# Optimization experiments

Measured on AMD Instinct MI355X. Metric: run time of the kernel, lower is better.

Reference implementation:

```python
import jax, jax.numpy as jnp
from jax import lax
import numpy as np

N_INPUTS = 256
N_REGS = 256
BATCH = 4096
T = 64  # num_clk_cycles


def setup_inputs() -> dict:
    key = jax.random.key(0)
    k1, k2, k3 = jax.random.split(key, 3)
    P = jax.random.normal(k1, (N_INPUTS, BATCH, T), dtype=jnp.float32)
    wa = jax.random.randint(k2, (N_REGS,), 0, N_INPUTS + N_REGS, dtype=jnp.int32)
    wb = jax.random.randint(k3, (N_REGS,), 0, N_INPUTS + N_REGS, dtype=jnp.int32)
    return {"P": P, "wa": wa, "wb": wb}


def reference(P, wa, wb):
    # PIEmbedding: clamp params to [-2,2], sigmoid(4*param[:, idx]) per cycle.
    # Precompute all cycles at once: X[t, b, i] in (0,1).
    X = jax.nn.sigmoid(4.0 * jnp.clip(P, -2.0, 2.0))          # [n_inputs, B, T]
    X = jnp.transpose(X, (2, 1, 0))                            # [T, B, n_inputs]
    B = P.shape[1]

    # Representative exec-generated soft sequential circuit:
    # each of N_REGS gates is a soft XOR of two signals drawn from
    # concat([primary_inputs, registers]); gate outputs become next registers.
    def step(states, x_t):
        sig = jnp.concatenate([x_t, states], axis=-1)          # [B, n_inputs+n_regs]
        a = sig[:, wa]                                          # [B, n_regs]
        b = sig[:, wb]
        new_states = a + b - 2.0 * a * b                        # soft XOR
        return new_states, None

    init = jnp.full((B, N_REGS), 0.5, dtype=P.dtype)            # init_registers()
    out, _ = lax.scan(step, init, X)                            # scan over clk cycles
    return out                                                  # [B, n_regs]
```

## Files before the change

kernel.cpp:

```cpp
#include <hip/hip_runtime.h>

#define N_IN   256
#define N_REG  256
#define NBATCH 4096
#define TT     64
#define TC     32
#define NCHUNK (TT / TC)
#define TILE_LD 257

__global__ __launch_bounds__(256, 4) void circuit_scan(
    const float* __restrict__ P,
    const int*   __restrict__ wa,
    const int*   __restrict__ wb,
    float*       __restrict__ out)
{
    __shared__ float tile[TC][TILE_LD];
    __shared__ float st0[N_REG];
    __shared__ float st1[N_REG];

    const int tid = threadIdx.x;
    const int b   = blockIdx.x;

    const int  ia   = wa[tid];
    const int  ib   = wb[tid];
    const bool a_in = ia < N_IN;
    const bool b_in = ib < N_IN;
    const int  ia_m = a_in ? ia : (ia - N_IN);
    const int  ib_m = b_in ? ib : (ib - N_IN);

    st0[tid] = 0.5f;

    const int row = tid >> 3;
    const int q   = tid & 7;

    float4 regs[8];

    #pragma unroll
    for (int it = 0; it < 8; ++it) {
        const int r = it * 32 + row;
        regs[it] = *reinterpret_cast<const float4*>(
            P + (size_t)r * (NBATCH * TT) + (size_t)b * TT + q * 4);
    }

    float mystate = 0.5f;

    for (int c = 0; c < NCHUNK; ++c) {
        #pragma unroll
        for (int it = 0; it < 8; ++it) {
            const int r = it * 32 + row;
            float xv[4] = {regs[it].x, regs[it].y, regs[it].z, regs[it].w};
            #pragma unroll
            for (int j = 0; j < 4; ++j) {
                float x = xv[j];
                x = fminf(2.0f, fmaxf(-2.0f, x));
                float s = 1.0f / (1.0f + __expf(-4.0f * x));
                tile[q * 4 + j][r] = s;
            }
        }
        if (c + 1 < NCHUNK) {
            const int t0 = (c + 1) * TC;
            #pragma unroll
            for (int it = 0; it < 8; ++it) {
                const int r = it * 32 + row;
                regs[it] = *reinterpret_cast<const float4*>(
                    P + (size_t)r * (NBATCH * TT) + (size_t)b * TT + t0 + q * 4);
            }
        }
        __syncthreads();

        #pragma unroll
        for (int tl = 0; tl < TC; ++tl) {
            const float* sread  = (tl & 1) ? st1 : st0;
            float*       swrite = (tl & 1) ? st0 : st1;
            const float* arow   = &tile[tl][0];
            float a  = *(a_in ? (arow + ia_m) : (sread + ia_m));
            float bb = *(b_in ? (arow + ib_m) : (sread + ib_m));
            float ns = a + bb - 2.0f * a * bb;
            swrite[tid] = ns;
            mystate = ns;
            __syncthreads();
        }
    }

    out[(size_t)b * N_REG + tid] = mystate;
}

extern "C" void kernel_launch(void* const* d_in, const int* in_sizes, int n_in,
                              void* d_out, int out_size, void* d_ws, size_t ws_size,
                              hipStream_t stream) {
    const float* P  = (const float*)d_in[0];
    const int*   wa = (const int*)d_in[1];
    const int*   wb = (const int*)d_in[2];
    float*       out = (float*)d_out;
    circuit_scan<<<NBATCH, 256, 0, stream>>>(P, wa, wb, out);
}
```

Baseline: 364.2 us.

## Run each batch row as a single wavefront to drop per-step barriers

Each batch element now gets one 64-lane wavefront instead of a 256-thread block, and each lane owns four registers. Because only one wave touches the shared state, the per-cycle __syncthreads and the double-buffered state arrays go away. Each step reads all old states before writing the new ones, so the update stays synchronous. The input tile is transposed to a padded [input][time] layout with per-lane pointers that advance each cycle, and the chunk size drops to 16. The cost is fewer threads per block and four times the serial work per lane. The design also relies on in-order LDS access within a wavefront instead of explicit barriers.

```diff
diff --git a/kernel.cpp b/kernel.cpp
--- a/kernel.cpp
+++ b/kernel.cpp
@@ -4,93 +4,109 @@
 #define N_REG  256
 #define NBATCH 4096
 #define TT     64
-#define TC     32
+#define TC     16
 #define NCHUNK (TT / TC)
-#define TILE_LD 257
+#define XT_LD  17
+#define ST_BASE (N_IN * XT_LD)
 
-__global__ __launch_bounds__(256, 4) void circuit_scan(
+__global__ __launch_bounds__(64, 2) void circuit_scan(
     const float* __restrict__ P,
     const int*   __restrict__ wa,
     const int*   __restrict__ wb,
     float*       __restrict__ out)
 {
-    __shared__ float tile[TC][TILE_LD];
-    __shared__ float st0[N_REG];
-    __shared__ float st1[N_REG];
+    __shared__ float lds[ST_BASE + N_REG];
 
-    const int tid = threadIdx.x;
-    const int b   = blockIdx.x;
+    const int lane = threadIdx.x;
+    const int b    = blockIdx.x;
+    const float* Pb = P + (size_t)b * TT;
 
-    const int  ia   = wa[tid];
-    const int  ib   = wb[tid];
-    const bool a_in = ia < N_IN;
-    const bool b_in = ib < N_IN;
-    const int  ia_m = a_in ? ia : (ia - N_IN);
-    const int  ib_m = b_in ? ib : (ib - N_IN);
-
-    st0[tid] = 0.5f;
-
-    const int row = tid >> 3;
-    const int q   = tid & 7;
-
-    float4 regs[8];
+    const float* pa0[4]; const float* pb0[4];
+    int inca[4], incb[4];
+    float sv[4];
 
     #pragma unroll
-    for (int it = 0; it < 8; ++it) {
-        const int r = it * 32 + row;
-        regs[it] = *reinterpret_cast<const float4*>(
-            P + (size_t)r * (NBATCH * TT) + (size_t)b * TT + q * 4);
+    for (int k = 0; k < 4; ++k) {
+        const int r  = lane + 64 * k;
+        const int ia = wa[r];
+        const int ib = wb[r];
+        const bool axk = ia < N_IN;
+        const bool bxk = ib < N_IN;
+        pa0[k] = lds + (axk ? ia * XT_LD : ST_BASE + (ia - N_IN));
+        pb0[k] = lds + (bxk ? ib * XT_LD : ST_BASE + (ib - N_IN));
+        inca[k] = axk ? 1 : 0;
+        incb[k] = bxk ? 1 : 0;
+        lds[ST_BASE + r] = 0.5f;
+        sv[k] = 0.5f;
     }
 
-    float mystate = 0.5f;
+    float4 pf[16];
+    #pragma unroll
+    for (int k2 = 0; k2 < 4; ++k2) {
+        const size_t rbase = (size_t)(lane + 64 * k2) * ((size_t)NBATCH * TT);
+        #pragma unroll
+        for (int q = 0; q < 4; ++q)
+            pf[k2 * 4 + q] = *reinterpret_cast<const float4*>(Pb + rbase + q * 4);
+    }
 
     for (int c = 0; c < NCHUNK; ++c) {
         #pragma unroll
-        for (int it = 0; it < 8; ++it) {
-            const int r = it * 32 + row;
-            float xv[4] = {regs[it].x, regs[it].y, regs[it].z, regs[it].w};
+        for (int k2 = 0; k2 < 4; ++k2) {
+            const int r = lane + 64 * k2;
             #pragma unroll
-            for (int j = 0; j < 4; ++j) {
-                float x = xv[j];
-                x = fminf(2.0f, fmaxf(-2.0f, x));
-                float s = 1.0f / (1.0f + __expf(-4.0f * x));
-                tile[q * 4 + j][r] = s;
+            for (int q = 0; q < 4; ++q) {
+                const float4 v = pf[k2 * 4 + q];
+                const float xs[4] = {v.x, v.y, v.z, v.w};
+                #pragma unroll
+                for (int j = 0; j < 4; ++j) {
+                    float x = fminf(2.0f, fmaxf(-2.0f, xs[j]));
+                    lds[r * XT_LD + 4 * q + j] = 1.0f / (1.0f + __expf(-4.0f * x));
+                }
             }
         }
         if (c + 1 < NCHUNK) {
-            const int t0 = (c + 1) * TC;
             #pragma unroll
-            for (int it = 0; it < 8; ++it) {
-                const int r = it * 32 + row;
-                regs[it] = *reinterpret_cast<const float4*>(
-                    P + (size_t)r * (NBATCH * TT) + (size_t)b * TT + t0 + q * 4);
+            for (int k2 = 0; k2 < 4; ++k2) {
+                const size_t rbase = (size_t)(lane + 64 * k2) * ((size_t)NBATCH * TT);
+                #pragma unroll
+                for (int q = 0; q < 4; ++q)
+                    pf[k2 * 4 + q] = *reinterpret_cast<const float4*>(
+                        Pb + rbase + (c + 1) * TC + q * 4);
             }
         }
-        __syncthreads();
+        const float* pa[4]; const float* pb[4];
+        #pragma unroll
+        for (int k = 0; k < 4; ++k) { pa[k] = pa0[k]; pb[k] = pb0[k]; }
 
         #pragma unroll
-        for (int tl = 0; tl < TC; ++tl) {
-            const float* sread  = (tl & 1) ? st1 : st0;
-            float*       swrite = (tl & 1) ? st0 : st1;
-            const float* arow   = &tile[tl][0];
-            float a  = *(a_in ? (arow + ia_m) : (sread + ia_m));
-            float bb = *(b_in ? (arow + ib_m) : (sread + ib_m));
-            float ns = a + bb - 2.0f * a * bb;
-            swrite[tid] = ns;
-            mystate = ns;
-            __syncthreads();
+        for (int t = 0; t < TC; ++t) {
+            float av[4], bv[4];
+            #pragma unroll
+            for (int k = 0; k < 4; ++k) { av[k] = *pa[k]; bv[k] = *pb[k]; }
+            #pragma unroll
+            for (int k = 0; k < 4; ++k) {
+                const float a  = av[k];
+                const float bb = bv[k];
+                const float ns = a + bb - 2.0f * a * bb;
+                sv[k] = ns;
+                lds[ST_BASE + lane + 64 * k] = ns;
+                pa[k] += inca[k];
+                pb[k] += incb[k];
+            }
         }
     }
 
-    out[(size_t)b * N_REG + tid] = mystate;
+    #pragma unroll
+    for (int k = 0; k < 4; ++k)
+        out[(size_t)b * N_REG + lane + 64 * k] = sv[k];
 }
 
 extern "C" void kernel_launch(void* const* d_in, const int* in_sizes, int n_in,
                               void* d_out, int out_size, void* d_ws, size_t ws_size,
                               hipStream_t stream) {
-    const float* P  = (const float*)d_in[0];
-    const int*   wa = (const int*)d_in[1];
-    const int*   wb = (const int*)d_in[2];
+    const float* P   = (const float*)d_in[0];
+    const int*   wa  = (const int*)d_in[1];
+    const int*   wb  = (const int*)d_in[2];
     float*       out = (float*)d_out;
-    circuit_scan<<<NBATCH, 256, 0, stream>>>(P, wa, wb, out);
+    circuit_scan<<<NBATCH, 64, 0, stream>>>(P, wa, wb, out);
 }
```

Measured after the change: 388.8 us. +6.7%, slower.
